# Optimization experiments

Hardware: AMD Instinct MI355X
Metric: run time of the kernel (lower is better)

Reference implementation:

```python
import jax, jax.numpy as jnp
import numpy as np

D_MODEL = 1024
N_HEADS = 16
HEAD_DIM = D_MODEL // N_HEADS
ROPE_THETA = 10000.0


def setup_inputs() -> dict:
    key = jax.random.key(0)
    ks = jax.random.split(key, 5)
    B, S = 4, 2048
    x = jax.random.normal(ks[0], (B, S, D_MODEL), dtype=jnp.float32)
    Wq = jax.random.normal(ks[1], (D_MODEL, D_MODEL), dtype=jnp.float32) * 0.02
    Wk = jax.random.normal(ks[2], (D_MODEL, D_MODEL), dtype=jnp.float32) * 0.02
    Wv = jax.random.normal(ks[3], (D_MODEL, D_MODEL), dtype=jnp.float32) * 0.02
    Wo = jax.random.normal(ks[4], (D_MODEL, D_MODEL), dtype=jnp.float32) * 0.02
    token_positions = jnp.arange(S, dtype=jnp.int32)
    return {"x": x, "token_positions": token_positions, "Wq": Wq, "Wk": Wk, "Wv": Wv, "Wo": Wo}


def apply_rope(t, positions):
    # t: [B, H, S, Dk]; positions: [S]
    half = HEAD_DIM // 2
    inv_freq = 1.0 / (ROPE_THETA ** (jnp.arange(half, dtype=jnp.float32) * 2.0 / HEAD_DIM))
    angles = positions.astype(jnp.float32)[:, None] * inv_freq[None, :]  # [S, half]
    cos = jnp.cos(angles)[None, None]  # [1,1,S,half]
    sin = jnp.sin(angles)[None, None]
    t_even = t[..., 0::2]
    t_odd = t[..., 1::2]
    rot_even = t_even * cos - t_odd * sin
    rot_odd = t_even * sin + t_odd * cos
    out = jnp.stack([rot_even, rot_odd], axis=-1)  # [B,H,S,half,2]
    return out.reshape(t.shape)


def reference(x, token_positions, Wq, Wk, Wv, Wo):
    B, S, _ = x.shape
    H, Dk = N_HEADS, HEAD_DIM
    # QKV projections, split heads -> [B, H, S, Dk]
    q = (x @ Wq).reshape(B, S, H, Dk).transpose(0, 2, 1, 3)
    k = (x @ Wk).reshape(B, S, H, Dk).transpose(0, 2, 1, 3)
    v = (x @ Wv).reshape(B, S, H, Dk).transpose(0, 2, 1, 3)
    q = apply_rope(q, token_positions)
    k = apply_rope(k, token_positions)
    scale = 1.0 / jnp.sqrt(jnp.asarray(Dk, dtype=x.dtype))
    scores = jnp.einsum('bhqd,bhkd->bhqk', q, k) * scale
    causal = jnp.tril(jnp.ones((S, S), dtype=bool))
    scores = jnp.where(causal[None, None], scores, jnp.asarray(-jnp.inf, dtype=scores.dtype))
    attn = jax.nn.softmax(scores, axis=-1)
    ctx = jnp.einsum('bhqk,bhkd->bhqd', attn, v)  # [B,H,S,Dk]
    ctx = ctx.transpose(0, 2, 1, 3).reshape(B, S, H * Dk)
    return ctx @ Wo
```

## Files before the change

kernel.cpp:

```cpp
#include <hip/hip_runtime.h>

typedef unsigned short u16;
typedef unsigned int   u32;
typedef __bf16  bf16x8 __attribute__((ext_vector_type(8)));
typedef float   f32x4  __attribute__((ext_vector_type(4)));
typedef float   f32x16 __attribute__((ext_vector_type(16)));
typedef u16     u16x4  __attribute__((ext_vector_type(4)));
typedef u16     u16x8  __attribute__((ext_vector_type(8)));
typedef u32     u32x4  __attribute__((ext_vector_type(4)));

#define D_MODEL 1024
#define N_HEADS 16
#define HEAD_DIM 64
#define BATCH 4
#define SEQ 2048
#define MROWS (BATCH*SEQ)

__device__ __forceinline__ u16 f2bf(float f){
  unsigned u = __builtin_bit_cast(unsigned, f);
  u += 0x7fffu + ((u >> 16) & 1u);
  return (u16)(u >> 16);
}
__device__ __forceinline__ float bf2f(u16 h){
  unsigned u = ((unsigned)h) << 16;
  return __builtin_bit_cast(float, u);
}
__device__ __forceinline__ u32 cvtpk(float a, float b){
  u32 r; asm("v_cvt_pk_bf16_f32 %0, %1, %2" : "=v"(r) : "v"(a), "v"(b)); return r;
}
__device__ __forceinline__ void gload_lds16(const u16* g, u16* l){
  __builtin_amdgcn_global_load_lds((const __attribute__((address_space(1))) void*)g,
                                   (__attribute__((address_space(3))) void*)l, 16, 0, 0);
}
#define MFMA16(a,b,c) __builtin_amdgcn_mfma_f32_16x16x32_bf16((a),(b),(c),0,0,0)

__global__ void k_cvt_x(const float* __restrict__ x, u16* __restrict__ xb, int n4){
  int i = blockIdx.x * 256 + threadIdx.x;
  if (i >= n4) return;
  float4 v = reinterpret_cast<const float4*>(x)[i];
  u16x4 o;
  o.x = f2bf(v.x); o.y = f2bf(v.y); o.z = f2bf(v.z); o.w = f2bf(v.w);
  *reinterpret_cast<u16x4*>(xb + (size_t)i * 4) = o;
}

__global__ void k_transpose_w(const float* __restrict__ Wq, const float* __restrict__ Wk,
                              const float* __restrict__ Wv, const float* __restrict__ Wo,
                              u16* __restrict__ wt){
  __shared__ float t[32][33];
  int z = blockIdx.z;
  const float* W = (z==0)?Wq:(z==1)?Wk:(z==2)?Wv:Wo;
  u16* O = wt + (size_t)z * (D_MODEL*(size_t)D_MODEL);
  int n0 = blockIdx.x*32, k0 = blockIdx.y*32;
  int tx = threadIdx.x, ty = threadIdx.y;
  #pragma unroll
  for (int i = ty; i < 32; i += 8) t[i][tx] = W[(size_t)(k0+i)*D_MODEL + n0 + tx];
  __syncthreads();
  #pragma unroll
  for (int i = ty; i < 32; i += 8){
    int n = n0 + i;
    int np = n;
    if (z < 2){ int d = n & 63; np = (n & ~63) | ((d & 1) << 5) | (d >> 1); }
    O[(size_t)np*D_MODEL + k0 + tx] = f2bf(t[tx][i]);
  }
}

__global__ void k_rope_tab(const int* __restrict__ pos, float2* __restrict__ tab){
  int i = blockIdx.x * 256 + threadIdx.x;
  int s = i >> 5, f = i & 31;
  float inv = exp2f(-(float)f * (13.287712379549449f / 32.0f));
  float a = (float)pos[s] * inv;
  float sn, cs;
  sincosf(a, &sn, &cs);
  tab[i] = make_float2(cs, sn);
}

__global__ __launch_bounds__(512, 4) void k_gqkv(const u16* __restrict__ A, const u16* __restrict__ Bt,
                                                 const float2* __restrict__ tab,
                                                 u16* __restrict__ qout, u16* __restrict__ kout,
                                                 u16* __restrict__ vout){
  __shared__ u16 sh[3*12288];
  const int tid = threadIdx.x, lane = tid & 63, w = tid >> 6;
  const int lr = lane & 15, lg = lane >> 4;
  const int m0 = blockIdx.x * 128, n0 = blockIdx.y * 256;
  const int wm = w >> 2, wn = w & 3;
  const int ra = tid >> 2;
  const int sca = ((tid & 3) ^ ((ra >> 1) & 3)) << 3;
  const u16* gA  = A  + (size_t)(m0 + ra)*1024 + sca;
  const u16* gB0 = Bt + (size_t)(n0 + ra)*1024 + sca;
  const int rb1 = 128 + ra;
  const u16* gB1 = Bt + (size_t)(n0 + rb1)*1024 + (((tid & 3) ^ ((rb1 >> 1) & 3)) << 3);
  const int dA  = w*512;
  const int dB0 = 4096 + w*512;
  const int dB1 = 8192 + w*512;
  int aoff[4], boff[4];
  #pragma unroll
  for (int mi = 0; mi < 4; ++mi){ int r_ = wm*64 + mi*16 + lr; aoff[mi] = r_*32 + ((lg ^ ((r_>>1)&3)) << 3); }
  #pragma unroll
  for (int ni = 0; ni < 4; ++ni){ int r_ = wn*64 + ni*16 + lr; boff[ni] = 4096 + r_*32 + ((lg ^ ((r_>>1)&3)) << 3); }

  f32x4 acc[4][4] = {};
#define SA_(base, t)  gload_lds16(gA  + (size_t)(t)*32, sh + (base) + dA)
#define SB0_(base, t) gload_lds16(gB0 + (size_t)(t)*32, sh + (base) + dB0)
#define SB1_(base, t) gload_lds16(gB1 + (size_t)(t)*32, sh + (base) + dB1)
  SA_(0,0); SB0_(0,0); SB1_(0,0);
  SA_(12288,1); SB0_(12288,1); SB1_(12288,1);
  int b0 = 0, b1 = 12288, b2 = 24576;
  #pragma unroll 1
  for (int t = 0; t < 32; ++t){
    if (t < 31) { asm volatile("s_waitcnt vmcnt(3) lgkmcnt(0)" ::: "memory"); }
    else        { asm volatile("s_waitcnt vmcnt(0) lgkmcnt(0)" ::: "memory"); }
    __builtin_amdgcn_s_barrier();
    __builtin_amdgcn_sched_barrier(0);
    const u16* Sb = sh + b0;
    bf16x8 af0 = *(const bf16x8*)&Sb[aoff[0]];
    bf16x8 af1 = *(const bf16x8*)&Sb[aoff[1]];
    bf16x8 af2 = *(const bf16x8*)&Sb[aoff[2]];
    bf16x8 af3 = *(const bf16x8*)&Sb[aoff[3]];
    bf16x8 vb0 = *(const bf16x8*)&Sb[boff[0]];
    bf16x8 vb1 = *(const bf16x8*)&Sb[boff[1]];
    if (t < 30){ SA_(b2, t+2); }
    __builtin_amdgcn_s_setprio(1);
    acc[0][0] = MFMA16(af0, vb0, acc[0][0]);
    acc[1][0] = MFMA16(af1, vb0, acc[1][0]);
    acc[2][0] = MFMA16(af2, vb0, acc[2][0]);
    acc[3][0] = MFMA16(af3, vb0, acc[3][0]);
    acc[0][1] = MFMA16(af0, vb1, acc[0][1]);
    acc[1][1] = MFMA16(af1, vb1, acc[1][1]);
    acc[2][1] = MFMA16(af2, vb1, acc[2][1]);
    acc[3][1] = MFMA16(af3, vb1, acc[3][1]);
    __builtin_amdgcn_s_setprio(0);
    bf16x8 vb2 = *(const bf16x8*)&Sb[boff[2]];
    bf16x8 vb3 = *(const bf16x8*)&Sb[boff[3]];
    if (t < 30){ SB0_(b2, t+2); SB1_(b2, t+2); }
    __builtin_amdgcn_s_setprio(1);
    acc[0][2] = MFMA16(af0, vb2, acc[0][2]);
    acc[1][2] = MFMA16(af1, vb2, acc[1][2]);
    acc[2][2] = MFMA16(af2, vb2, acc[2][2]);
    acc[3][2] = MFMA16(af3, vb2, acc[3][2]);
    acc[0][3] = MFMA16(af0, vb3, acc[0][3]);
    acc[1][3] = MFMA16(af1, vb3, acc[1][3]);
    acc[2][3] = MFMA16(af2, vb3, acc[2][3]);
    acc[3][3] = MFMA16(af3, vb3, acc[3][3]);
    __builtin_amdgcn_s_setprio(0);
    int tmp = b0; b0 = b1; b1 = b2; b2 = tmp;
  }
#undef SA_
#undef SB0_
#undef SB1_

  const int which = n0 >> 10;
  #pragma unroll
  for (int mi = 0; mi < 4; mi++){
    int row = m0 + wm*64 + mi*16 + lg*4;
    #pragma unroll
    for (int ni = 0; ni < 4; ni++){
      int col = n0 + wn*64 + ni*16 + lr;
      int cm = col & 1023;
      int hh = cm >> 6, d = cm & 63;
      f32x4 vv = acc[mi][ni];
      f32x4 vp = acc[mi][ni ^ 2];
      #pragma unroll
      for (int r = 0; r < 4; r++){
        int rr = row + r;
        int bb = rr >> 11, s = rr & (SEQ-1);
        float val = vv[r];
        if (which < 2){
          float e = (ni < 2) ? val : vp[r];
          float o = (ni < 2) ? vp[r] : val;
          float2 cs = tab[s*32 + ((ni & 1) << 4) + lr];
          float ov = (ni < 2) ? (e*cs.x - o*cs.y) : (e*cs.y + o*cs.x);
          if (which == 0){
            ov *= 0.18033688011112042f;
            qout[(size_t)rr*1024 + cm] = f2bf(ov);
          } else {
            kout[(((size_t)(bb*N_HEADS + hh))*SEQ + s)*64 + d] = f2bf(ov);
          }
        } else {
          vout[(((size_t)(bb*N_HEADS + hh))*(SEQ/16) + (s >> 4))*1024 + d*16 + (s & 15)] = f2bf(val);
        }
      }
    }
  }
}

__global__ __launch_bounds__(256, 4) void k_gwo(const u16* __restrict__ A, const u16* __restrict__ Bt,
                                                float* __restrict__ fout){
  __shared__ u16 sh[3*8192];
  const int tid = threadIdx.x, lane = tid & 63, w = tid >> 6;
  const int lr = lane & 15, lg = lane >> 4;
  const int m0 = blockIdx.x * 128, n0 = blockIdx.y * 128;
  const int wm = w >> 1, wn = w & 1;
  const int ra = w*16 + (lane >> 2);
  const int sc = ((lane & 3) ^ ((ra >> 1) & 3)) << 3;
  const u16* gA0 = A  + (size_t)(m0 + ra)*1024 + sc;
  const u16* gA1 = A  + (size_t)(m0 + 64 + ra)*1024 + sc;
  const u16* gB0 = Bt + (size_t)(n0 + ra)*1024 + sc;
  const u16* gB1 = Bt + (size_t)(n0 + 64 + ra)*1024 + sc;
  int aoff[4], boff[4];
  #pragma unroll
  for (int mi = 0; mi < 4; ++mi){ int r_ = wm*64 + mi*16 + lr; aoff[mi] = r_*32 + ((lg ^ ((r_>>1)&3)) << 3); }
  #pragma unroll
  for (int ni = 0; ni < 4; ++ni){ int r_ = wn*64 + ni*16 + lr; boff[ni] = 4096 + r_*32 + ((lg ^ ((r_>>1)&3)) << 3); }
  f32x4 acc[4][4] = {};
#define SAW(base, t) { gload_lds16(gA0 + (size_t)(t)*32, sh + (base) + w*512); \
                       gload_lds16(gA1 + (size_t)(t)*32, sh + (base) + 2048 + w*512); }
#define SBW(base, t) { gload_lds16(gB0 + (size_t)(t)*32, sh + (base) + 4096 + w*512); \
                       gload_lds16(gB1 + (size_t)(t)*32, sh + (base) + 6144 + w*512); }
  SAW(0,0) SBW(0,0)
  SAW(8192,1) SBW(8192,1)
  int b0 = 0, b1 = 8192, b2 = 16384;
  #pragma unroll 1
  for (int t = 0; t < 32; ++t){
    if (t < 31) { asm volatile("s_waitcnt vmcnt(4) lgkmcnt(0)" ::: "memory"); }
    else        { asm volatile("s_waitcnt vmcnt(0) lgkmcnt(0)" ::: "memory"); }
    __builtin_amdgcn_s_barrier();
    __builtin_amdgcn_sched_barrier(0);
    const u16* Sb = sh + b0;
    bf16x8 af0 = *(const bf16x8*)&Sb[aoff[0]];
    bf16x8 af1 = *(const bf16x8*)&Sb[aoff[1]];
    bf16x8 af2 = *(const bf16x8*)&Sb[aoff[2]];
    bf16x8 af3 = *(const bf16x8*)&Sb[aoff[3]];
    bf16x8 vb0 = *(const bf16x8*)&Sb[boff[0]];
    bf16x8 vb1 = *(const bf16x8*)&Sb[boff[1]];
    if (t < 30){ SAW(b2, t+2) }
    __builtin_amdgcn_s_setprio(1);
    acc[0][0] = MFMA16(af0, vb0, acc[0][0]);
    acc[1][0] = MFMA16(af1, vb0, acc[1][0]);
    acc[2][0] = MFMA16(af2, vb0, acc[2][0]);
    acc[3][0] = MFMA16(af3, vb0, acc[3][0]);
    acc[0][1] = MFMA16(af0, vb1, acc[0][1]);
    acc[1][1] = MFMA16(af1, vb1, acc[1][1]);
    acc[2][1] = MFMA16(af2, vb1, acc[2][1]);
    acc[3][1] = MFMA16(af3, vb1, acc[3][1]);
    __builtin_amdgcn_s_setprio(0);
    bf16x8 vb2 = *(const bf16x8*)&Sb[boff[2]];
    bf16x8 vb3 = *(const bf16x8*)&Sb[boff[3]];
    if (t < 30){ SBW(b2, t+2) }
    __builtin_amdgcn_s_setprio(1);
    acc[0][2] = MFMA16(af0, vb2, acc[0][2]);
    acc[1][2] = MFMA16(af1, vb2, acc[1][2]);
    acc[2][2] = MFMA16(af2, vb2, acc[2][2]);
    acc[3][2] = MFMA16(af3, vb2, acc[3][2]);
    acc[0][3] = MFMA16(af0, vb3, acc[0][3]);
    acc[1][3] = MFMA16(af1, vb3, acc[1][3]);
    acc[2][3] = MFMA16(af2, vb3, acc[2][3]);
    acc[3][3] = MFMA16(af3, vb3, acc[3][3]);
    __builtin_amdgcn_s_setprio(0);
    int tmp = b0; b0 = b1; b1 = b2; b2 = tmp;
  }
#undef SAW
#undef SBW
  #pragma unroll
  for (int mi = 0; mi < 4; mi++){
    int row = m0 + wm*64 + mi*16 + lg*4;
    #pragma unroll
    for (int ni = 0; ni < 4; ni++){
      int col = n0 + wn*64 + ni*16 + lr;
      f32x4 vv = acc[mi][ni];
      #pragma unroll
      for (int r = 0; r < 4; r++)
        fout[(size_t)(row + r)*1024 + col] = vv[r];
    }
  }
}

__global__ __launch_bounds__(256, 3) void k_attn(const u16* __restrict__ q, const u16* __restrict__ k2,
                                                 const u16* __restrict__ v2, u16* __restrict__ ctx){
  __shared__ u16 kv[2][8192];
  const int lane = threadIdx.x & 63, w = threadIdx.x >> 6;
  const int lq = lane & 31, hl = lane >> 5;
  const int B = blockIdx.x;
  const int bh = B & 63, g = 15 - (B >> 6);
  const int b = bh >> 4, h = bh & 15;
  const int qi = 4*g + w;
  const int q0 = qi * 32;
  const int qmax0 = (4*g + 3) * 32;
  const u16* kglob = k2 + (size_t)bh*SEQ*64;
  const u16* vglob = v2 + (size_t)bh*(SEQ/16)*1024;

  const u16* qr_ = q + (size_t)(b*SEQ + q0 + lq)*D_MODEL + h*HEAD_DIM + hl*8;
  bf16x8 qf0 = *(const bf16x8*)&qr_[0];
  bf16x8 qf1 = *(const bf16x8*)&qr_[16];
  bf16x8 qf2 = *(const bf16x8*)&qr_[32];
  bf16x8 qf3 = *(const bf16x8*)&qr_[48];
  f32x16 acc0 = {}, acc1 = {};
  float m = -3.0e38f, l = 0.f;

  const int kr_ = (w<<3) + (lane>>3);
  const int kc_ = ((lane&7) ^ (lane>>3)) << 3;
  auto STAGE = [&](int bf, int jt){
    gload_lds16(kglob + (size_t)(jt      + kr_)*64 + kc_, &kv[bf][w<<9]);
    gload_lds16(kglob + (size_t)(jt + 32 + kr_)*64 + kc_, &kv[bf][2048 + (w<<9)]);
    gload_lds16(vglob + ((size_t)(jt>>4)<<10)        + (w<<9) + (lane<<3), &kv[bf][4096 + (w<<9)]);
    gload_lds16(vglob + ((size_t)((jt+32)>>4)<<10)   + (w<<9) + (lane<<3), &kv[bf][6144 + (w<<9)]);
  };

  STAGE(0, 0);
  __syncthreads();
  int p = 0;
  for (int j0 = 0; j0 <= qmax0; j0 += 64){
    if (j0 + 64 <= qmax0) STAGE(p^1, j0 + 64);
    if (j0 <= q0){
      const bool g2 = (j0 + 32 <= q0);
      const char* kb = (const char*)&kv[p][0];
      f32x16 S1 = {};
      {
        bf16x8 kf0 = *(const bf16x8*)(kb + lq*128 + (((0+hl) ^ (lq&7))<<4));
        bf16x8 kf1 = *(const bf16x8*)(kb + lq*128 + (((2+hl) ^ (lq&7))<<4));
        bf16x8 kf2 = *(const bf16x8*)(kb + lq*128 + (((4+hl) ^ (lq&7))<<4));
        bf16x8 kf3 = *(const bf16x8*)(kb + lq*128 + (((6+hl) ^ (lq&7))<<4));
        S1 = __builtin_amdgcn_mfma_f32_32x32x16_bf16(kf0, qf0, S1, 0, 0, 0);
        S1 = __builtin_amdgcn_mfma_f32_32x32x16_bf16(kf1, qf1, S1, 0, 0, 0);
        S1 = __builtin_amdgcn_mfma_f32_32x32x16_bf16(kf2, qf2, S1, 0, 0, 0);
        S1 = __builtin_amdgcn_mfma_f32_32x32x16_bf16(kf3, qf3, S1, 0, 0, 0);
      }
      if (j0 == q0){
        #pragma unroll
        for (int r = 0; r < 16; ++r){
          int kk = (r & 3) + 8*(r >> 2) + 4*hl;
          if (kk > lq) S1[r] = -3.0e38f;
        }
      }
      f32x16 S2 = {};
      if (g2){
        const char* kb2 = kb + 4096;
        bf16x8 kf0 = *(const bf16x8*)(kb2 + lq*128 + (((0+hl) ^ (lq&7))<<4));
        bf16x8 kf1 = *(const bf16x8*)(kb2 + lq*128 + (((2+hl) ^ (lq&7))<<4));
        bf16x8 kf2 = *(const bf16x8*)(kb2 + lq*128 + (((4+hl) ^ (lq&7))<<4));
        bf16x8 kf3 = *(const bf16x8*)(kb2 + lq*128 + (((6+hl) ^ (lq&7))<<4));
        S2 = __builtin_amdgcn_mfma_f32_32x32x16_bf16(kf0, qf0, S2, 0, 0, 0);
        S2 = __builtin_amdgcn_mfma_f32_32x32x16_bf16(kf1, qf1, S2, 0, 0, 0);
        S2 = __builtin_amdgcn_mfma_f32_32x32x16_bf16(kf2, qf2, S2, 0, 0, 0);
        S2 = __builtin_amdgcn_mfma_f32_32x32x16_bf16(kf3, qf3, S2, 0, 0, 0);
        if (j0 + 32 == q0){
          #pragma unroll
          for (int r = 0; r < 16; ++r){
            int kk = (r & 3) + 8*(r >> 2) + 4*hl;
            if (kk > lq) S2[r] = -3.0e38f;
          }
        }
      }
      float pm = fmaxf(fmaxf(fmaxf(S1[0],S1[1]), fmaxf(S1[2],S1[3])),
                       fmaxf(fmaxf(S1[4],S1[5]), fmaxf(S1[6],S1[7])));
      pm = fmaxf(pm, fmaxf(fmaxf(fmaxf(S1[8],S1[9]), fmaxf(S1[10],S1[11])),
                           fmaxf(fmaxf(S1[12],S1[13]),fmaxf(S1[14],S1[15]))));
      if (g2){
        float pm2 = fmaxf(fmaxf(fmaxf(S2[0],S2[1]), fmaxf(S2[2],S2[3])),
                          fmaxf(fmaxf(S2[4],S2[5]), fmaxf(S2[6],S2[7])));
        pm2 = fmaxf(pm2, fmaxf(fmaxf(fmaxf(S2[8],S2[9]), fmaxf(S2[10],S2[11])),
                               fmaxf(fmaxf(S2[12],S2[13]),fmaxf(S2[14],S2[15]))));
        pm = fmaxf(pm, pm2);
      }
      pm = fmaxf(pm, __shfl_xor(pm, 32));
      if (__any(pm > m + 8.f)){
        float mn = fmaxf(m, pm);
        float cr = __builtin_amdgcn_exp2f(m - mn);
        l *= cr;
        #pragma unroll
        for (int r = 0; r < 16; ++r){ acc0[r] *= cr; acc1[r] *= cr; }
        m = mn;
      }
      #pragma unroll
      for (int r = 0; r < 16; ++r) S1[r] = __builtin_amdgcn_exp2f(S1[r] - m);
      l += ((S1[0]+S1[1])+(S1[2]+S1[3])) + ((S1[4]+S1[5])+(S1[6]+S1[7]))
         + ((S1[8]+S1[9])+(S1[10]+S1[11])) + ((S1[12]+S1[13])+(S1[14]+S1[15]));
      {
        u32 g0a = cvtpk(S1[0], S1[1]),  g0b = cvtpk(S1[2], S1[3]);
        u32 g1a = cvtpk(S1[4], S1[5]),  g1b = cvtpk(S1[6], S1[7]);
        u32 g2a = cvtpk(S1[8], S1[9]),  g2b = cvtpk(S1[10],S1[11]);
        u32 g3a = cvtpk(S1[12],S1[13]), g3b = cvtpk(S1[14],S1[15]);
        u32 s0a = hl ? g0a : g1a, s0b = hl ? g0b : g1b;
        u32 e0a = (u32)__shfl_xor((int)s0a, 32), e0b = (u32)__shfl_xor((int)s0b, 32);
        u32 m0a = hl ? g1a : g0a, m0b = hl ? g1b : g0b;
        u32 s1a = hl ? g2a : g3a, s1b = hl ? g2b : g3b;
        u32 e1a = (u32)__shfl_xor((int)s1a, 32), e1b = (u32)__shfl_xor((int)s1b, 32);
        u32 m1a = hl ? g3a : g2a, m1b = hl ? g3b : g2b;
        u32x4 A0 = { hl ? e0a : m0a, hl ? e0b : m0b, hl ? m0a : e0a, hl ? m0b : e0b };
        u32x4 A1 = { hl ? e1a : m1a, hl ? e1b : m1b, hl ? m1a : e1a, hl ? m1b : e1b };
        bf16x8 pa0 = __builtin_bit_cast(bf16x8, A0);
        bf16x8 pa1 = __builtin_bit_cast(bf16x8, A1);
        const char* vb = kb + 8192;
        bf16x8 vf00 = *(const bf16x8*)(vb + lq*32 + hl*16);
        bf16x8 vf01 = *(const bf16x8*)(vb + lq*32 + hl*16 + 1024);
        bf16x8 vf10 = *(const bf16x8*)(vb + lq*32 + hl*16 + 2048);
        bf16x8 vf11 = *(const bf16x8*)(vb + lq*32 + hl*16 + 3072);
        acc0 = __builtin_amdgcn_mfma_f32_32x32x16_bf16(vf00, pa0, acc0, 0, 0, 0);
        acc0 = __builtin_amdgcn_mfma_f32_32x32x16_bf16(vf10, pa1, acc0, 0, 0, 0);
        acc1 = __builtin_amdgcn_mfma_f32_32x32x16_bf16(vf01, pa0, acc1, 0, 0, 0);
        acc1 = __builtin_amdgcn_mfma_f32_32x32x16_bf16(vf11, pa1, acc1, 0, 0, 0);
      }
      if (g2){
        #pragma unroll
        for (int r = 0; r < 16; ++r) S2[r] = __builtin_amdgcn_exp2f(S2[r] - m);
        l += ((S2[0]+S2[1])+(S2[2]+S2[3])) + ((S2[4]+S2[5])+(S2[6]+S2[7]))
           + ((S2[8]+S2[9])+(S2[10]+S2[11])) + ((S2[12]+S2[13])+(S2[14]+S2[15]));
        u32 g0a = cvtpk(S2[0], S2[1]),  g0b = cvtpk(S2[2], S2[3]);
        u32 g1a = cvtpk(S2[4], S2[5]),  g1b = cvtpk(S2[6], S2[7]);
        u32 g2a_ = cvtpk(S2[8], S2[9]), g2b_ = cvtpk(S2[10],S2[11]);
        u32 g3a = cvtpk(S2[12],S2[13]), g3b = cvtpk(S2[14],S2[15]);
        u32 s0a = hl ? g0a : g1a, s0b = hl ? g0b : g1b;
        u32 e0a = (u32)__shfl_xor((int)s0a, 32), e0b = (u32)__shfl_xor((int)s0b, 32);
        u32 m0a = hl ? g1a : g0a, m0b = hl ? g1b : g0b;
        u32 s1a = hl ? g2a_ : g3a, s1b = hl ? g2b_ : g3b;
        u32 e1a = (u32)__shfl_xor((int)s1a, 32), e1b = (u32)__shfl_xor((int)s1b, 32);
        u32 m1a = hl ? g3a : g2a_, m1b = hl ? g3b : g2b_;
        u32x4 A0 = { hl ? e0a : m0a, hl ? e0b : m0b, hl ? m0a : e0a, hl ? m0b : e0b };
        u32x4 A1 = { hl ? e1a : m1a, hl ? e1b : m1b, hl ? m1a : e1a, hl ? m1b : e1b };
        bf16x8 pa0 = __builtin_bit_cast(bf16x8, A0);
        bf16x8 pa1 = __builtin_bit_cast(bf16x8, A1);
        const char* vb = kb + 12288;
        bf16x8 vf00 = *(const bf16x8*)(vb + lq*32 + hl*16);
        bf16x8 vf01 = *(const bf16x8*)(vb + lq*32 + hl*16 + 1024);
        bf16x8 vf10 = *(const bf16x8*)(vb + lq*32 + hl*16 + 2048);
        bf16x8 vf11 = *(const bf16x8*)(vb + lq*32 + hl*16 + 3072);
        acc0 = __builtin_amdgcn_mfma_f32_32x32x16_bf16(vf00, pa0, acc0, 0, 0, 0);
        acc0 = __builtin_amdgcn_mfma_f32_32x32x16_bf16(vf10, pa1, acc0, 0, 0, 0);
        acc1 = __builtin_amdgcn_mfma_f32_32x32x16_bf16(vf01, pa0, acc1, 0, 0, 0);
        acc1 = __builtin_amdgcn_mfma_f32_32x32x16_bf16(vf11, pa1, acc1, 0, 0, 0);
      }
    }
    __syncthreads();
    p ^= 1;
  }
  l += __shfl_xor(l, 32);
  float inv = __builtin_amdgcn_rcpf(l);
  char* tbc = (char*)kv + w*4096;
  #pragma unroll
  for (int r = 0; r < 16; ++r){
    int d0 = (r & 3) + 8*(r >> 2) + 4*hl;
    *(u16*)(tbc + lq*128 + ((2*d0)      ^ ((lq & 7) << 4))) = f2bf(acc0[r] * inv);
    *(u16*)(tbc + lq*128 + ((2*(d0+32)) ^ ((lq & 7) << 4))) = f2bf(acc1[r] * inv);
  }
  int qr2 = lane >> 1, chb = (lane & 1) * 4;
  u16* cp = ctx + (size_t)(b*SEQ + q0 + qr2)*D_MODEL + h*HEAD_DIM;
  #pragma unroll
  for (int i = 0; i < 4; ++i){
    int ch = chb + i;
    u16x8 vv = *(const u16x8*)(tbc + qr2*128 + 16*(ch ^ (qr2 & 7)));
    *(u16x8*)&cp[ch*8] = vv;
  }
}

extern "C" void kernel_launch(void* const* d_in, const int* in_sizes, int n_in,
                              void* d_out, int out_size, void* d_ws, size_t ws_size,
                              hipStream_t stream){
  const float* x  = (const float*)d_in[0];
  const int*  pos = (const int*)d_in[1];
  const float* Wq = (const float*)d_in[2];
  const float* Wk = (const float*)d_in[3];
  const float* Wv = (const float*)d_in[4];
  const float* Wo = (const float*)d_in[5];
  float* out = (float*)d_out;
  char* ws = (char*)d_ws;
  u16* xb   = (u16*)(ws);
  u16* wt   = (u16*)(ws + 16777216);
  u16* qb   = (u16*)(ws + 25165824);
  u16* kbh  = (u16*)(ws + 41943040);
  u16* vt2  = (u16*)(ws + 58720256);
  float2* tab = (float2*)(ws + 75497472);
  u16* ctxb = xb;

  k_cvt_x<<<(MROWS*D_MODEL/4)/256, 256, 0, stream>>>(x, xb, MROWS*D_MODEL/4);
  k_transpose_w<<<dim3(32,32,4), dim3(32,8), 0, stream>>>(Wq, Wk, Wv, Wo, wt);
  k_rope_tab<<<(SEQ*32)/256, 256, 0, stream>>>(pos, tab);
  k_gqkv<<<dim3(64,12), 512, 0, stream>>>(xb, wt, tab, qb, kbh, vt2);
  k_attn<<<dim3(1024), 256, 0, stream>>>(qb, kbh, vt2, ctxb);
  k_gwo<<<dim3(64,8), 256, 0, stream>>>(ctxb, wt + 3145728, out);
}
```

Baseline: 179.9 us.

## Unify QKV and output GEMMs into one 256x256-tile kernel with 4-stage pipeline

Both projection GEMMs now use a single templated kernel with 256x256 output tiles (8x4 MFMA tiles per wave), a four-buffer LDS ring with three tiles prefetched ahead, and a mid-iteration barrier between the two halves. Larger tiles raise operand reuse per byte loaded and the deeper pipeline is meant to hide global latency. In exchange, occupancy drops to 2 blocks per CU with 128KB of LDS per block. The grids shrink a lot: 384 blocks for QKV and only 128 for Wo, which may leave many of the 256 CUs idle.

```diff
diff --git a/kernel.cpp b/kernel.cpp
--- a/kernel.cpp
+++ b/kernel.cpp
@@ -74,192 +74,115 @@
   tab[i] = make_float2(cs, sn);
 }
 
-__global__ __launch_bounds__(512, 4) void k_gqkv(const u16* __restrict__ A, const u16* __restrict__ Bt,
+template<int MODE>
+__global__ __launch_bounds__(512, 2) void k_g256(const u16* __restrict__ A, const u16* __restrict__ Bt,
                                                  const float2* __restrict__ tab,
                                                  u16* __restrict__ qout, u16* __restrict__ kout,
-                                                 u16* __restrict__ vout){
-  __shared__ u16 sh[3*12288];
+                                                 u16* __restrict__ vout, float* __restrict__ fout){
+  __shared__ u16 sh[4*16384];
   const int tid = threadIdx.x, lane = tid & 63, w = tid >> 6;
   const int lr = lane & 15, lg = lane >> 4;
-  const int m0 = blockIdx.x * 128, n0 = blockIdx.y * 256;
+  const int m0 = blockIdx.x * 256, n0 = blockIdx.y * 256;
   const int wm = w >> 2, wn = w & 3;
-  const int ra = tid >> 2;
-  const int sca = ((tid & 3) ^ ((ra >> 1) & 3)) << 3;
-  const u16* gA  = A  + (size_t)(m0 + ra)*1024 + sca;
-  const u16* gB0 = Bt + (size_t)(n0 + ra)*1024 + sca;
-  const int rb1 = 128 + ra;
-  const u16* gB1 = Bt + (size_t)(n0 + rb1)*1024 + (((tid & 3) ^ ((rb1 >> 1) & 3)) << 3);
-  const int dA  = w*512;
-  const int dB0 = 4096 + w*512;
-  const int dB1 = 8192 + w*512;
-  int aoff[4], boff[4];
-  #pragma unroll
-  for (int mi = 0; mi < 4; ++mi){ int r_ = wm*64 + mi*16 + lr; aoff[mi] = r_*32 + ((lg ^ ((r_>>1)&3)) << 3); }
-  #pragma unroll
-  for (int ni = 0; ni < 4; ++ni){ int r_ = wn*64 + ni*16 + lr; boff[ni] = 4096 + r_*32 + ((lg ^ ((r_>>1)&3)) << 3); }
-
-  f32x4 acc[4][4] = {};
-#define SA_(base, t)  gload_lds16(gA  + (size_t)(t)*32, sh + (base) + dA)
-#define SB0_(base, t) gload_lds16(gB0 + (size_t)(t)*32, sh + (base) + dB0)
-#define SB1_(base, t) gload_lds16(gB1 + (size_t)(t)*32, sh + (base) + dB1)
-  SA_(0,0); SB0_(0,0); SB1_(0,0);
-  SA_(12288,1); SB0_(12288,1); SB1_(12288,1);
-  int b0 = 0, b1 = 12288, b2 = 24576;
+  const int r_  = tid >> 2;
+  const int c_  = ((tid & 3) ^ ((r_  >> 1) & 3)) << 3;
+  const int r1_ = 128 + r_;
+  const int c1_ = ((tid & 3) ^ ((r1_ >> 1) & 3)) << 3;
+  const u16* gA0 = A  + (size_t)(m0 + r_ )*1024 + c_;
+  const u16* gA1 = A  + (size_t)(m0 + r1_)*1024 + c1_;
+  const u16* gB0 = Bt + (size_t)(n0 + r_ )*1024 + c_;
+  const u16* gB1 = Bt + (size_t)(n0 + r1_)*1024 + c1_;
+  int aoff[8], boff[4];
+  #pragma unroll
+  for (int mi = 0; mi < 8; ++mi){ int r = wm*128 + mi*16 + lr; aoff[mi] = r*32 + ((lg ^ ((r>>1)&3)) << 3); }
+  #pragma unroll
+  for (int ni = 0; ni < 4; ++ni){ int r = wn*64 + ni*16 + lr; boff[ni] = 8192 + r*32 + ((lg ^ ((r>>1)&3)) << 3); }
+
+  f32x4 acc[8][4] = {};
+#define STGA(buf, t) { u16* D = sh + (buf)*16384 + (w<<9); \
+    gload_lds16(gA0 + (size_t)(t)*32, D); \
+    gload_lds16(gA1 + (size_t)(t)*32, D + 4096); }
+#define STGB(buf, t) { u16* D = sh + (buf)*16384 + 8192 + (w<<9); \
+    gload_lds16(gB0 + (size_t)(t)*32, D); \
+    gload_lds16(gB1 + (size_t)(t)*32, D + 4096); }
+
+  STGA(0,0) STGB(0,0)
+  STGA(1,1) STGB(1,1)
+  STGA(2,2) STGB(2,2)
   #pragma unroll 1
   for (int t = 0; t < 32; ++t){
-    if (t < 31) { asm volatile("s_waitcnt vmcnt(3) lgkmcnt(0)" ::: "memory"); }
-    else        { asm volatile("s_waitcnt vmcnt(0) lgkmcnt(0)" ::: "memory"); }
+    if (t < 30)       { asm volatile("s_waitcnt vmcnt(8)" ::: "memory"); }
+    else if (t == 30) { asm volatile("s_waitcnt vmcnt(4)" ::: "memory"); }
+    else              { asm volatile("s_waitcnt vmcnt(0)" ::: "memory"); }
     __builtin_amdgcn_s_barrier();
     __builtin_amdgcn_sched_barrier(0);
-    const u16* Sb = sh + b0;
-    bf16x8 af0 = *(const bf16x8*)&Sb[aoff[0]];
-    bf16x8 af1 = *(const bf16x8*)&Sb[aoff[1]];
-    bf16x8 af2 = *(const bf16x8*)&Sb[aoff[2]];
-    bf16x8 af3 = *(const bf16x8*)&Sb[aoff[3]];
-    bf16x8 vb0 = *(const bf16x8*)&Sb[boff[0]];
-    bf16x8 vb1 = *(const bf16x8*)&Sb[boff[1]];
-    if (t < 30){ SA_(b2, t+2); }
+    const u16* Sb = sh + (t & 3)*16384;
+    const int ts = t + 3, bs = ts & 3;
+    bf16x8 bf_[4], af[4];
+    #pragma unroll
+    for (int ni = 0; ni < 4; ++ni) bf_[ni] = *(const bf16x8*)&Sb[boff[ni]];
+    #pragma unroll
+    for (int mi = 0; mi < 4; ++mi) af[mi] = *(const bf16x8*)&Sb[aoff[mi]];
+    if (t < 29){ STGA(bs, ts) }
     __builtin_amdgcn_s_setprio(1);
-    acc[0][0] = MFMA16(af0, vb0, acc[0][0]);
-    acc[1][0] = MFMA16(af1, vb0, acc[1][0]);
-    acc[2][0] = MFMA16(af2, vb0, acc[2][0]);
-    acc[3][0] = MFMA16(af3, vb0, acc[3][0]);
-    acc[0][1] = MFMA16(af0, vb1, acc[0][1]);
-    acc[1][1] = MFMA16(af1, vb1, acc[1][1]);
-    acc[2][1] = MFMA16(af2, vb1, acc[2][1]);
-    acc[3][1] = MFMA16(af3, vb1, acc[3][1]);
+    #pragma unroll
+    for (int mi = 0; mi < 4; ++mi)
+      #pragma unroll
+      for (int ni = 0; ni < 4; ++ni)
+        acc[mi][ni] = MFMA16(af[mi], bf_[ni], acc[mi][ni]);
     __builtin_amdgcn_s_setprio(0);
-    bf16x8 vb2 = *(const bf16x8*)&Sb[boff[2]];
-    bf16x8 vb3 = *(const bf16x8*)&Sb[boff[3]];
-    if (t < 30){ SB0_(b2, t+2); SB1_(b2, t+2); }
+    __builtin_amdgcn_s_barrier();
+    #pragma unroll
+    for (int mi = 0; mi < 4; ++mi) af[mi] = *(const bf16x8*)&Sb[aoff[4+mi]];
+    if (t < 29){ STGB(bs, ts) }
     __builtin_amdgcn_s_setprio(1);
-    acc[0][2] = MFMA16(af0, vb2, acc[0][2]);
-    acc[1][2] = MFMA16(af1, vb2, acc[1][2]);
-    acc[2][2] = MFMA16(af2, vb2, acc[2][2]);
-    acc[3][2] = MFMA16(af3, vb2, acc[3][2]);
-    acc[0][3] = MFMA16(af0, vb3, acc[0][3]);
-    acc[1][3] = MFMA16(af1, vb3, acc[1][3]);
-    acc[2][3] = MFMA16(af2, vb3, acc[2][3]);
-    acc[3][3] = MFMA16(af3, vb3, acc[3][3]);
+    #pragma unroll
+    for (int mi = 0; mi < 4; ++mi)
+      #pragma unroll
+      for (int ni = 0; ni < 4; ++ni)
+        acc[4+mi][ni] = MFMA16(af[mi], bf_[ni], acc[4+mi][ni]);
     __builtin_amdgcn_s_setprio(0);
-    int tmp = b0; b0 = b1; b1 = b2; b2 = tmp;
-  }
-#undef SA_
-#undef SB0_
-#undef SB1_
+  }
+#undef STGA
+#undef STGB
 
   const int which = n0 >> 10;
   #pragma unroll
-  for (int mi = 0; mi < 4; mi++){
-    int row = m0 + wm*64 + mi*16 + lg*4;
-    #pragma unroll
-    for (int ni = 0; ni < 4; ni++){
-      int col = n0 + wn*64 + ni*16 + lr;
-      int cm = col & 1023;
-      int hh = cm >> 6, d = cm & 63;
-      f32x4 vv = acc[mi][ni];
-      f32x4 vp = acc[mi][ni ^ 2];
-      #pragma unroll
-      for (int r = 0; r < 4; r++){
-        int rr = row + r;
-        int bb = rr >> 11, s = rr & (SEQ-1);
-        float val = vv[r];
-        if (which < 2){
-          float e = (ni < 2) ? val : vp[r];
-          float o = (ni < 2) ? vp[r] : val;
-          float2 cs = tab[s*32 + ((ni & 1) << 4) + lr];
-          float ov = (ni < 2) ? (e*cs.x - o*cs.y) : (e*cs.y + o*cs.x);
-          if (which == 0){
-            ov *= 0.18033688011112042f;
-            qout[(size_t)rr*1024 + cm] = f2bf(ov);
-          } else {
-            kout[(((size_t)(bb*N_HEADS + hh))*SEQ + s)*64 + d] = f2bf(ov);
-          }
-        } else {
-          vout[(((size_t)(bb*N_HEADS + hh))*(SEQ/16) + (s >> 4))*1024 + d*16 + (s & 15)] = f2bf(val);
-        }
-      }
-    }
-  }
-}
-
-__global__ __launch_bounds__(256, 4) void k_gwo(const u16* __restrict__ A, const u16* __restrict__ Bt,
-                                                float* __restrict__ fout){
-  __shared__ u16 sh[3*8192];
-  const int tid = threadIdx.x, lane = tid & 63, w = tid >> 6;
-  const int lr = lane & 15, lg = lane >> 4;
-  const int m0 = blockIdx.x * 128, n0 = blockIdx.y * 128;
-  const int wm = w >> 1, wn = w & 1;
-  const int ra = w*16 + (lane >> 2);
-  const int sc = ((lane & 3) ^ ((ra >> 1) & 3)) << 3;
-  const u16* gA0 = A  + (size_t)(m0 + ra)*1024 + sc;
-  const u16* gA1 = A  + (size_t)(m0 + 64 + ra)*1024 + sc;
-  const u16* gB0 = Bt + (size_t)(n0 + ra)*1024 + sc;
-  const u16* gB1 = Bt + (size_t)(n0 + 64 + ra)*1024 + sc;
-  int aoff[4], boff[4];
-  #pragma unroll
-  for (int mi = 0; mi < 4; ++mi){ int r_ = wm*64 + mi*16 + lr; aoff[mi] = r_*32 + ((lg ^ ((r_>>1)&3)) << 3); }
-  #pragma unroll
-  for (int ni = 0; ni < 4; ++ni){ int r_ = wn*64 + ni*16 + lr; boff[ni] = 4096 + r_*32 + ((lg ^ ((r_>>1)&3)) << 3); }
-  f32x4 acc[4][4] = {};
-#define SAW(base, t) { gload_lds16(gA0 + (size_t)(t)*32, sh + (base) + w*512); \
-                       gload_lds16(gA1 + (size_t)(t)*32, sh + (base) + 2048 + w*512); }
-#define SBW(base, t) { gload_lds16(gB0 + (size_t)(t)*32, sh + (base) + 4096 + w*512); \
-                       gload_lds16(gB1 + (size_t)(t)*32, sh + (base) + 6144 + w*512); }
-  SAW(0,0) SBW(0,0)
-  SAW(8192,1) SBW(8192,1)
-  int b0 = 0, b1 = 8192, b2 = 16384;
-  #pragma unroll 1
-  for (int t = 0; t < 32; ++t){
-    if (t < 31) { asm volatile("s_waitcnt vmcnt(4) lgkmcnt(0)" ::: "memory"); }
-    else        { asm volatile("s_waitcnt vmcnt(0) lgkmcnt(0)" ::: "memory"); }
-    __builtin_amdgcn_s_barrier();
-    __builtin_amdgcn_sched_barrier(0);
-    const u16* Sb = sh + b0;
-    bf16x8 af0 = *(const bf16x8*)&Sb[aoff[0]];
-    bf16x8 af1 = *(const bf16x8*)&Sb[aoff[1]];
-    bf16x8 af2 = *(const bf16x8*)&Sb[aoff[2]];
-    bf16x8 af3 = *(const bf16x8*)&Sb[aoff[3]];
-    bf16x8 vb0 = *(const bf16x8*)&Sb[boff[0]];
-    bf16x8 vb1 = *(const bf16x8*)&Sb[boff[1]];
-    if (t < 30){ SAW(b2, t+2) }
-    __builtin_amdgcn_s_setprio(1);
-    acc[0][0] = MFMA16(af0, vb0, acc[0][0]);
-    acc[1][0] = MFMA16(af1, vb0, acc[1][0]);
-    acc[2][0] = MFMA16(af2, vb0, acc[2][0]);
-    acc[3][0] = MFMA16(af3, vb0, acc[3][0]);
-    acc[0][1] = MFMA16(af0, vb1, acc[0][1]);
-    acc[1][1] = MFMA16(af1, vb1, acc[1][1]);
-    acc[2][1] = MFMA16(af2, vb1, acc[2][1]);
-    acc[3][1] = MFMA16(af3, vb1, acc[3][1]);
-    __builtin_amdgcn_s_setprio(0);
-    bf16x8 vb2 = *(const bf16x8*)&Sb[boff[2]];
-    bf16x8 vb3 = *(const bf16x8*)&Sb[boff[3]];
-    if (t < 30){ SBW(b2, t+2) }
-    __builtin_amdgcn_s_setprio(1);
-    acc[0][2] = MFMA16(af0, vb2, acc[0][2]);
-    acc[1][2] = MFMA16(af1, vb2, acc[1][2]);
-    acc[2][2] = MFMA16(af2, vb2, acc[2][2]);
-    acc[3][2] = MFMA16(af3, vb2, acc[3][2]);
-    acc[0][3] = MFMA16(af0, vb3, acc[0][3]);
-    acc[1][3] = MFMA16(af1, vb3, acc[1][3]);
-    acc[2][3] = MFMA16(af2, vb3, acc[2][3]);
-    acc[3][3] = MFMA16(af3, vb3, acc[3][3]);
-    __builtin_amdgcn_s_setprio(0);
-    int tmp = b0; b0 = b1; b1 = b2; b2 = tmp;
-  }
-#undef SAW
-#undef SBW
-  #pragma unroll
-  for (int mi = 0; mi < 4; mi++){
-    int row = m0 + wm*64 + mi*16 + lg*4;
+  for (int mi = 0; mi < 8; mi++){
+    int row = m0 + wm*128 + mi*16 + lg*4;
     #pragma unroll
     for (int ni = 0; ni < 4; ni++){
       int col = n0 + wn*64 + ni*16 + lr;
       f32x4 vv = acc[mi][ni];
-      #pragma unroll
-      for (int r = 0; r < 4; r++)
-        fout[(size_t)(row + r)*1024 + col] = vv[r];
+      if (MODE == 1){
+        #pragma unroll
+        for (int r = 0; r < 4; r++)
+          fout[(size_t)(row + r)*1024 + col] = vv[r];
+      } else {
+        int cm = col & 1023;
+        int hh = cm >> 6, d = cm & 63;
+        f32x4 vp = acc[mi][ni ^ 2];
+        #pragma unroll
+        for (int r = 0; r < 4; r++){
+          int rr = row + r;
+          int bb = rr >> 11, s = rr & (SEQ-1);
+          float val = vv[r];
+          if (which < 2){
+            float e = (ni < 2) ? val : vp[r];
+            float o = (ni < 2) ? vp[r] : val;
+            float2 cs = tab[s*32 + ((ni & 1) << 4) + lr];
+            float ov = (ni < 2) ? (e*cs.x - o*cs.y) : (e*cs.y + o*cs.x);
+            if (which == 0){
+              ov *= 0.18033688011112042f;
+              qout[(size_t)rr*1024 + cm] = f2bf(ov);
+            } else {
+              kout[(((size_t)(bb*N_HEADS + hh))*SEQ + s)*64 + d] = f2bf(ov);
+            }
+          } else {
+            vout[(((size_t)(bb*N_HEADS + hh))*(SEQ/16) + (s >> 4))*1024 + d*16 + (s & 15)] = f2bf(val);
+          }
+        }
+      }
     }
   }
 }
@@ -463,7 +386,7 @@
   k_cvt_x<<<(MROWS*D_MODEL/4)/256, 256, 0, stream>>>(x, xb, MROWS*D_MODEL/4);
   k_transpose_w<<<dim3(32,32,4), dim3(32,8), 0, stream>>>(Wq, Wk, Wv, Wo, wt);
   k_rope_tab<<<(SEQ*32)/256, 256, 0, stream>>>(pos, tab);
-  k_gqkv<<<dim3(64,12), 512, 0, stream>>>(xb, wt, tab, qb, kbh, vt2);
+  k_g256<0><<<dim3(32,12), 512, 0, stream>>>(xb, wt, tab, qb, kbh, vt2, nullptr);
   k_attn<<<dim3(1024), 256, 0, stream>>>(qb, kbh, vt2, ctxb);
-  k_gwo<<<dim3(64,8), 256, 0, stream>>>(ctxb, wt + 3145728, out);
-}
+  k_g256<1><<<dim3(32,4), 512, 0, stream>>>(ctxb, wt + 3145728, nullptr, nullptr, nullptr, nullptr, out);
+}
```

Result: slower. 219.9 us (+22.2%).

## Use 4-wave QKV GEMM blocks with 128x64 per-wave tiles

Applied to the files above, without the earlier changes.

The fused QKV projection GEMM now runs with 256 threads (4 waves) per block instead of 512. Each wave covers all 128 rows and a 64-column strip, giving 8x4 MFMA accumulators per wave, and each thread issues twice as many global-to-LDS copies. The intent is to raise the MFMA-to-LDS-read ratio per wave and cut barrier and wave overhead. In exchange, register pressure per wave roughly doubles and there are fewer waves to hide latency.

```diff
diff --git a/kernel.cpp b/kernel.cpp
--- a/kernel.cpp
+++ b/kernel.cpp
@@ -74,87 +74,82 @@
   tab[i] = make_float2(cs, sn);
 }
 
-__global__ __launch_bounds__(512, 4) void k_gqkv(const u16* __restrict__ A, const u16* __restrict__ Bt,
-                                                 const float2* __restrict__ tab,
-                                                 u16* __restrict__ qout, u16* __restrict__ kout,
-                                                 u16* __restrict__ vout){
+__global__ __launch_bounds__(256, 2) void k_gq4(const u16* __restrict__ A, const u16* __restrict__ Bt,
+                                                const float2* __restrict__ tab,
+                                                u16* __restrict__ qout, u16* __restrict__ kout,
+                                                u16* __restrict__ vout){
   __shared__ u16 sh[3*12288];
   const int tid = threadIdx.x, lane = tid & 63, w = tid >> 6;
   const int lr = lane & 15, lg = lane >> 4;
   const int m0 = blockIdx.x * 128, n0 = blockIdx.y * 256;
-  const int wm = w >> 2, wn = w & 3;
-  const int ra = tid >> 2;
-  const int sca = ((tid & 3) ^ ((ra >> 1) & 3)) << 3;
-  const u16* gA  = A  + (size_t)(m0 + ra)*1024 + sca;
-  const u16* gB0 = Bt + (size_t)(n0 + ra)*1024 + sca;
-  const int rb1 = 128 + ra;
-  const u16* gB1 = Bt + (size_t)(n0 + rb1)*1024 + (((tid & 3) ^ ((rb1 >> 1) & 3)) << 3);
-  const int dA  = w*512;
-  const int dB0 = 4096 + w*512;
-  const int dB1 = 8192 + w*512;
-  int aoff[4], boff[4];
-  #pragma unroll
-  for (int mi = 0; mi < 4; ++mi){ int r_ = wm*64 + mi*16 + lr; aoff[mi] = r_*32 + ((lg ^ ((r_>>1)&3)) << 3); }
-  #pragma unroll
-  for (int ni = 0; ni < 4; ++ni){ int r_ = wn*64 + ni*16 + lr; boff[ni] = 4096 + r_*32 + ((lg ^ ((r_>>1)&3)) << 3); }
-
-  f32x4 acc[4][4] = {};
-#define SA_(base, t)  gload_lds16(gA  + (size_t)(t)*32, sh + (base) + dA)
-#define SB0_(base, t) gload_lds16(gB0 + (size_t)(t)*32, sh + (base) + dB0)
-#define SB1_(base, t) gload_lds16(gB1 + (size_t)(t)*32, sh + (base) + dB1)
-  SA_(0,0); SB0_(0,0); SB1_(0,0);
-  SA_(12288,1); SB0_(12288,1); SB1_(12288,1);
+  const int sr = lane >> 2;
+  const int rA0 = (w*2+0)*16 + sr, rA1 = (w*2+1)*16 + sr;
+  const u16* gA0 = A + (size_t)(m0 + rA0)*1024 + (((lane&3) ^ ((rA0>>1)&3))<<3);
+  const u16* gA1 = A + (size_t)(m0 + rA1)*1024 + (((lane&3) ^ ((rA1>>1)&3))<<3);
+  const int rB0 = (w*4+0)*16 + sr, rB1 = (w*4+1)*16 + sr, rB2 = (w*4+2)*16 + sr, rB3 = (w*4+3)*16 + sr;
+  const u16* gB0 = Bt + (size_t)(n0 + rB0)*1024 + (((lane&3) ^ ((rB0>>1)&3))<<3);
+  const u16* gB1 = Bt + (size_t)(n0 + rB1)*1024 + (((lane&3) ^ ((rB1>>1)&3))<<3);
+  const u16* gB2 = Bt + (size_t)(n0 + rB2)*1024 + (((lane&3) ^ ((rB2>>1)&3))<<3);
+  const u16* gB3 = Bt + (size_t)(n0 + rB3)*1024 + (((lane&3) ^ ((rB3>>1)&3))<<3);
+  int aoff[8], boff[4];
+  #pragma unroll
+  for (int mi = 0; mi < 8; ++mi){ int r = mi*16 + lr;        aoff[mi] = r*32 + ((lg ^ ((r>>1)&3)) << 3); }
+  #pragma unroll
+  for (int ni = 0; ni < 4; ++ni){ int r = w*64 + ni*16 + lr; boff[ni] = 4096 + r*32 + ((lg ^ ((r>>1)&3)) << 3); }
+
+  f32x4 acc[8][4] = {};
+#define STGA(base, t) { gload_lds16(gA0 + (size_t)(t)*32, sh + (base) + (w*2+0)*512); \
+                        gload_lds16(gA1 + (size_t)(t)*32, sh + (base) + (w*2+1)*512); }
+#define STGB(base, t) { gload_lds16(gB0 + (size_t)(t)*32, sh + (base) + 4096 + (w*4+0)*512); \
+                        gload_lds16(gB1 + (size_t)(t)*32, sh + (base) + 4096 + (w*4+1)*512); \
+                        gload_lds16(gB2 + (size_t)(t)*32, sh + (base) + 4096 + (w*4+2)*512); \
+                        gload_lds16(gB3 + (size_t)(t)*32, sh + (base) + 4096 + (w*4+3)*512); }
+
+  STGA(0,0) STGB(0,0)
+  STGA(12288,1) STGB(12288,1)
   int b0 = 0, b1 = 12288, b2 = 24576;
   #pragma unroll 1
   for (int t = 0; t < 32; ++t){
-    if (t < 31) { asm volatile("s_waitcnt vmcnt(3) lgkmcnt(0)" ::: "memory"); }
+    if (t < 31) { asm volatile("s_waitcnt vmcnt(6) lgkmcnt(0)" ::: "memory"); }
     else        { asm volatile("s_waitcnt vmcnt(0) lgkmcnt(0)" ::: "memory"); }
     __builtin_amdgcn_s_barrier();
     __builtin_amdgcn_sched_barrier(0);
     const u16* Sb = sh + b0;
-    bf16x8 af0 = *(const bf16x8*)&Sb[aoff[0]];
-    bf16x8 af1 = *(const bf16x8*)&Sb[aoff[1]];
-    bf16x8 af2 = *(const bf16x8*)&Sb[aoff[2]];
-    bf16x8 af3 = *(const bf16x8*)&Sb[aoff[3]];
-    bf16x8 vb0 = *(const bf16x8*)&Sb[boff[0]];
-    bf16x8 vb1 = *(const bf16x8*)&Sb[boff[1]];
-    if (t < 30){ SA_(b2, t+2); }
+    bf16x8 bf_[4], af[4];
+    #pragma unroll
+    for (int ni = 0; ni < 4; ++ni) bf_[ni] = *(const bf16x8*)&Sb[boff[ni]];
+    #pragma unroll
+    for (int mi = 0; mi < 4; ++mi) af[mi] = *(const bf16x8*)&Sb[aoff[mi]];
+    if (t < 30){ STGA(b2, t+2) }
     __builtin_amdgcn_s_setprio(1);
-    acc[0][0] = MFMA16(af0, vb0, acc[0][0]);
-    acc[1][0] = MFMA16(af1, vb0, acc[1][0]);
-    acc[2][0] = MFMA16(af2, vb0, acc[2][0]);
-    acc[3][0] = MFMA16(af3, vb0, acc[3][0]);
-    acc[0][1] = MFMA16(af0, vb1, acc[0][1]);
-    acc[1][1] = MFMA16(af1, vb1, acc[1][1]);
-    acc[2][1] = MFMA16(af2, vb1, acc[2][1]);
-    acc[3][1] = MFMA16(af3, vb1, acc[3][1]);
+    #pragma unroll
+    for (int mi = 0; mi < 4; ++mi)
+      #pragma unroll
+      for (int ni = 0; ni < 4; ++ni)
+        acc[mi][ni] = MFMA16(af[mi], bf_[ni], acc[mi][ni]);
     __builtin_amdgcn_s_setprio(0);
-    bf16x8 vb2 = *(const bf16x8*)&Sb[boff[2]];
-    bf16x8 vb3 = *(const bf16x8*)&Sb[boff[3]];
-    if (t < 30){ SB0_(b2, t+2); SB1_(b2, t+2); }
+    #pragma unroll
+    for (int mi = 0; mi < 4; ++mi) af[mi] = *(const bf16x8*)&Sb[aoff[4+mi]];
+    if (t < 30){ STGB(b2, t+2) }
     __builtin_amdgcn_s_setprio(1);
-    acc[0][2] = MFMA16(af0, vb2, acc[0][2]);
-    acc[1][2] = MFMA16(af1, vb2, acc[1][2]);
-    acc[2][2] = MFMA16(af2, vb2, acc[2][2]);
-    acc[3][2] = MFMA16(af3, vb2, acc[3][2]);
-    acc[0][3] = MFMA16(af0, vb3, acc[0][3]);
-    acc[1][3] = MFMA16(af1, vb3, acc[1][3]);
-    acc[2][3] = MFMA16(af2, vb3, acc[2][3]);
-    acc[3][3] = MFMA16(af3, vb3, acc[3][3]);
+    #pragma unroll
+    for (int mi = 0; mi < 4; ++mi)
+      #pragma unroll
+      for (int ni = 0; ni < 4; ++ni)
+        acc[4+mi][ni] = MFMA16(af[mi], bf_[ni], acc[4+mi][ni]);
     __builtin_amdgcn_s_setprio(0);
     int tmp = b0; b0 = b1; b1 = b2; b2 = tmp;
   }
-#undef SA_
-#undef SB0_
-#undef SB1_
+#undef STGA
+#undef STGB
 
   const int which = n0 >> 10;
   #pragma unroll
-  for (int mi = 0; mi < 4; mi++){
-    int row = m0 + wm*64 + mi*16 + lg*4;
+  for (int mi = 0; mi < 8; mi++){
+    int row = m0 + mi*16 + lg*4;
     #pragma unroll
     for (int ni = 0; ni < 4; ni++){
-      int col = n0 + wn*64 + ni*16 + lr;
+      int col = n0 + w*64 + ni*16 + lr;
       int cm = col & 1023;
       int hh = cm >> 6, d = cm & 63;
       f32x4 vv = acc[mi][ni];
@@ -463,7 +458,7 @@
   k_cvt_x<<<(MROWS*D_MODEL/4)/256, 256, 0, stream>>>(x, xb, MROWS*D_MODEL/4);
   k_transpose_w<<<dim3(32,32,4), dim3(32,8), 0, stream>>>(Wq, Wk, Wv, Wo, wt);
   k_rope_tab<<<(SEQ*32)/256, 256, 0, stream>>>(pos, tab);
-  k_gqkv<<<dim3(64,12), 512, 0, stream>>>(xb, wt, tab, qb, kbh, vt2);
+  k_gq4<<<dim3(64,12), 256, 0, stream>>>(xb, wt, tab, qb, kbh, vt2);
   k_attn<<<dim3(1024), 256, 0, stream>>>(qb, kbh, vt2, ctxb);
   k_gwo<<<dim3(64,8), 256, 0, stream>>>(ctxb, wt + 3145728, out);
 }
```

New measurement: 189.8 us. 1.05x slower.
